# Optimization experiments

Hardware: AMD Instinct MI355X
Metric: run time of the kernel (lower is better)

The kernel has to match this reference:

```python
import jax, jax.numpy as jnp
import numpy as np

D_MODEL = 1024
N_HEAD = 8
STRIDE = 8
HEAD_DIM = D_MODEL // N_HEAD
NEG_INF = jnp.float32(-1e30)  # stand-in for -inf, safe under softmax


def setup_inputs() -> dict:
    key = jax.random.key(0)
    ks = jax.random.split(key, 8)
    B, TGT, SRC = 2, 1024, 8192
    scale = 1.0 / np.sqrt(D_MODEL)
    return {
        "q": jax.random.normal(ks[0], (B, TGT, D_MODEL), jnp.float32),
        "k": jax.random.normal(ks[1], (B, SRC, D_MODEL), jnp.float32),
        "v": jax.random.normal(ks[2], (B, SRC, D_MODEL), jnp.float32),
        "Wq": jax.random.normal(ks[3], (D_MODEL, D_MODEL), jnp.float32) * scale,
        "bq": jnp.zeros((D_MODEL,), jnp.float32),
        "Wk": jax.random.normal(ks[4], (D_MODEL, D_MODEL), jnp.float32) * scale,
        "bk": jnp.zeros((D_MODEL,), jnp.float32),
        "Wv": jax.random.normal(ks[5], (D_MODEL, D_MODEL), jnp.float32) * scale,
        "bv": jnp.zeros((D_MODEL,), jnp.float32),
        "Wo": jax.random.normal(ks[6], (D_MODEL, D_MODEL), jnp.float32) * scale,
        "bo": jnp.zeros((D_MODEL,), jnp.float32),
    }


def _hepos_head_mask(src_len):
    # mask_h[h, j] True where position j is DISALLOWED for head h:
    # (j - h) % stride != 0. If a head would mask everything, unmask j=0
    # (matches the torch fallback; cannot happen when n_head <= stride... it
    # can when h >= stride? here h < n_head <= stride handled generically).
    src_idx = jnp.arange(src_len)  # [src]
    h_idx = jnp.arange(N_HEAD)[:, None]  # [H,1]
    m = ((src_idx[None, :] - h_idx) % STRIDE) != 0  # [H, src]
    all_masked = jnp.all(m, axis=-1, keepdims=True)  # [H,1]
    m = m.at[:, 0].set(jnp.where(all_masked[:, 0], False, m[:, 0]))
    return m


def reference(q, k, v, Wq, bq, Wk, bk, Wv, bv, Wo, bo):
    B, tgt_len, _ = q.shape
    src_len = k.shape[1]
    # projections (torch Linear: x @ W^T + b; here W stored as [d_in, d_out])
    Q = (q @ Wq + bq).reshape(B, tgt_len, N_HEAD, HEAD_DIM)
    K = (k @ Wk + bk).reshape(B, src_len, N_HEAD, HEAD_DIM)
    V = (v @ Wv + bv).reshape(B, src_len, N_HEAD, HEAD_DIM)
    # dense scores [B, H, tgt, src]
    scores = jnp.einsum('bthd,bshd->bhts', Q, K) / np.sqrt(HEAD_DIM)
    head_mask = _hepos_head_mask(src_len)  # [H, src], True -> disallowed
    scores = jnp.where(head_mask[None, :, None, :], NEG_INF, scores)
    attn = jax.nn.softmax(scores, axis=-1)
    out = jnp.einsum('bhts,bshd->bthd', attn, V).reshape(B, tgt_len, D_MODEL)
    return out @ Wo + bo
```

## Files before the change

kernel.cpp:

```cpp
#include <hip/hip_runtime.h>
#include <hip/hip_bf16.h>
#include <stdint.h>

#define DM 1024
#define HD 128
#define NH 8
#define NB 2
#define TGT 1024
#define SRC 8192
#define JPH 1024
#define LOG2E 1.4426950408889634f

typedef __attribute__((ext_vector_type(8))) short bf16x8;
typedef __attribute__((ext_vector_type(4))) float f32x4;

__device__ __forceinline__ unsigned short f2bf(float f) {
  __hip_bfloat16 h = __float2bfloat16(f);
  return __builtin_bit_cast(unsigned short, h);
}

__device__ __forceinline__ void gload_lds16(const void* g, void* l) {
  __builtin_amdgcn_global_load_lds(
      (const __attribute__((address_space(1))) unsigned int*)g,
      (__attribute__((address_space(3))) unsigned int*)l, 16, 0, 0);
}

__global__ __launch_bounds__(256) void wconv_kernel(
    const float* __restrict__ Wq, const float* __restrict__ Wk,
    const float* __restrict__ Wv, const float* __restrict__ Wo,
    unsigned short* __restrict__ WTout) {
  __shared__ float tile[64][65];
  const float* W = (blockIdx.z == 0) ? Wq : (blockIdx.z == 1) ? Wk
                   : (blockIdx.z == 2) ? Wv : Wo;
  unsigned short* WT = WTout + (size_t)blockIdx.z * DM * DM;
  const int k0 = blockIdx.x * 64, n0 = blockIdx.y * 64;
  const int tid = threadIdx.x;
  const int tr = tid >> 4, tc = (tid & 15) * 4;
  for (int it = 0; it < 4; ++it) {
    int r = tr + it * 16;
    float4 vv = *(const float4*)(&W[(size_t)(k0 + r) * DM + n0 + tc]);
    tile[r][tc] = vv.x; tile[r][tc + 1] = vv.y;
    tile[r][tc + 2] = vv.z; tile[r][tc + 3] = vv.w;
  }
  __syncthreads();
  for (int it = 0; it < 4; ++it) {
    int n = tr + it * 16;
    ushort4 o;
    o.x = f2bf(tile[tc + 0][n]); o.y = f2bf(tile[tc + 1][n]);
    o.z = f2bf(tile[tc + 2][n]); o.w = f2bf(tile[tc + 3][n]);
    *(ushort4*)(&WT[(size_t)(n0 + n) * DM + k0 + tc]) = o;
  }
}

__global__ __launch_bounds__(256) void proj_fused_kernel(
    const float* __restrict__ q, const float* __restrict__ k,
    const float* __restrict__ v, const unsigned short* __restrict__ WTall,
    const float* __restrict__ bq, const float* __restrict__ bk,
    const float* __restrict__ bv, unsigned short* __restrict__ Qp,
    unsigned short* __restrict__ Kp, unsigned short* __restrict__ VpT) {
  __shared__ unsigned short Ab[2][128 * 64];
  __shared__ unsigned short Bb[2][128 * 64];
  const int tid = threadIdx.x, lane = tid & 63, w = tid >> 6;
  const int wm = w >> 1, wn = w & 1;
  const int l15 = lane & 15, l4 = lane >> 4;

  const int bid = blockIdx.x;
  const int mode = bid >> 7;
  const int sub = bid & 127;
  const float* Asrc;
  const unsigned short* WT;
  const float* bias;
  int nbase, bh = 0, Mtile;
  if (mode == 0) {
    Asrc = q; WT = WTall; bias = bq;
    Mtile = sub >> 3; nbase = (sub & 7) * 128;
  } else {
    bh = sub >> 3; Mtile = sub & 7;
    nbase = (bh & 7) * 128;
    if (mode == 1) { Asrc = k; WT = WTall + (size_t)DM * DM; bias = bk; }
    else           { Asrc = v; WT = WTall + (size_t)2 * DM * DM; bias = bv; }
  }

  float4 areg[4][2];
  auto loadA = [&](int t) {
    const int kk0 = t * 64;
    for (int p = 0; p < 4; ++p) {
      int r = p * 32 + (tid >> 3);
      size_t grow;
      if (mode == 0) grow = (size_t)(Mtile * 128 + r);
      else grow = (size_t)(bh >> 3) * SRC + (size_t)(bh & 7) +
                  8u * (size_t)(Mtile * 128 + r);
      const float* src = &Asrc[grow * DM + kk0 + (tid & 7) * 8];
      areg[p][0] = *(const float4*)(src);
      areg[p][1] = *(const float4*)(src + 4);
    }
  };
  auto writeA = [&](int buf) {
    for (int p = 0; p < 4; ++p) {
      int r = p * 32 + (tid >> 3);
      bf16x8 pk;
      pk[0] = (short)f2bf(areg[p][0].x); pk[1] = (short)f2bf(areg[p][0].y);
      pk[2] = (short)f2bf(areg[p][0].z); pk[3] = (short)f2bf(areg[p][0].w);
      pk[4] = (short)f2bf(areg[p][1].x); pk[5] = (short)f2bf(areg[p][1].y);
      pk[6] = (short)f2bf(areg[p][1].z); pk[7] = (short)f2bf(areg[p][1].w);
      int off = r * 128 + (((tid & 7) * 16) ^ ((r & 7) << 4));
      *(bf16x8*)((unsigned char*)Ab[buf] + off) = pk;
    }
  };
  auto stageB = [&](int t, int buf) {
    const int kk0 = t * 64;
    for (int it = 0; it < 4; ++it) {
      int gi = w * 4 + it;
      int row = gi * 8 + (lane >> 3);
      const unsigned char* g =
          (const unsigned char*)&WT[(size_t)(nbase + row) * DM + kk0];
      g += ((lane & 7) * 16) ^ ((row & 7) << 4);
      gload_lds16(g, (unsigned char*)Bb[buf] + gi * 1024);
    }
  };

  f32x4 acc[4][4] = {};

  loadA(0);
  stageB(0, 0);
  writeA(0);
  __syncthreads();

  for (int t = 0; t < 16; ++t) {
    const int cur = t & 1;
    if (t < 15) { loadA(t + 1); stageB(t + 1, cur ^ 1); }

    bf16x8 af[4][2], bfr[4][2];
    for (int f = 0; f < 4; ++f)
      for (int kk = 0; kk < 2; ++kk) {
        int ra = wm * 64 + f * 16 + l15;
        int ka = (kk * 64 + l4 * 16) ^ ((ra & 7) << 4);
        af[f][kk] = *(const bf16x8*)((const unsigned char*)Ab[cur] + ra * 128 + ka);
        int rb = wn * 64 + f * 16 + l15;
        int kb = (kk * 64 + l4 * 16) ^ ((rb & 7) << 4);
        bfr[f][kk] = *(const bf16x8*)((const unsigned char*)Bb[cur] + rb * 128 + kb);
      }
    for (int kk = 0; kk < 2; ++kk)
      for (int fm = 0; fm < 4; ++fm)
        for (int fn = 0; fn < 4; ++fn)
          acc[fm][fn] = __builtin_amdgcn_mfma_f32_16x16x32_bf16(
              af[fm][kk], bfr[fn][kk], acc[fm][fn], 0, 0, 0);

    if (t < 15) writeA(cur ^ 1);
    __syncthreads();
  }

  for (int fm = 0; fm < 4; ++fm) {
    for (int fn = 0; fn < 4; ++fn) {
      const int mloc = wm * 64 + fm * 16 + l4 * 4;
      const int nloc = wn * 64 + fn * 16 + l15;
      const float bs = bias[nbase + nloc];
      if (mode == 2) {
        const int d = nloc;
        const int jp = Mtile * 128 + mloc;
        ushort4 o;
        o.x = f2bf(acc[fm][fn][0] + bs); o.y = f2bf(acc[fm][fn][1] + bs);
        o.z = f2bf(acc[fm][fn][2] + bs); o.w = f2bf(acc[fm][fn][3] + bs);
        *(ushort4*)(&VpT[((size_t)bh * HD + d) * JPH + jp]) = o;
      } else if (mode == 1) {
        for (int i = 0; i < 4; ++i) {
          int jp = Mtile * 128 + mloc + i;
          Kp[((size_t)bh * JPH + jp) * HD + nloc] = f2bf(acc[fm][fn][i] + bs);
        }
      } else {
        for (int i = 0; i < 4; ++i) {
          int mg = Mtile * 128 + mloc + i;
          int bb = mg >> 10, tt = mg & 1023;
          int ng = nbase + nloc;
          int h = ng >> 7, d = ng & 127;
          Qp[(((size_t)bb * NH + h) * TGT + tt) * HD + d] =
              f2bf((acc[fm][fn][i] + bs) * 0.08838834764831845f);
        }
      }
    }
  }
}

__global__ __launch_bounds__(256) void attn_kernel(
    const unsigned short* __restrict__ Qp, const unsigned short* __restrict__ Kp,
    const unsigned short* __restrict__ VpT, unsigned short* __restrict__ O) {
  __shared__ unsigned short Klds[64 * 128];
  __shared__ unsigned short Vlds[128 * 64];
  __shared__ unsigned short Plds[4 * 16 * 64];
  const int tid = threadIdx.x, lane = tid & 63, w = tid >> 6;
  const int tq = blockIdx.x, bh = blockIdx.y;
  const int T0 = tq * 64 + w * 16;
  const int l15 = lane & 15, l4 = lane >> 4;

  bf16x8 qf[4];
  {
    const unsigned short* qrow = &Qp[((size_t)bh * TGT + T0 + l15) * HD];
    for (int kf = 0; kf < 4; ++kf)
      qf[kf] = *(const bf16x8*)(&qrow[kf * 32 + l4 * 8]);
  }

  f32x4 acc_o[8] = {};
  float m_run = -INFINITY, l_run = 0.f;

  const unsigned short* kbh = Kp + (size_t)bh * JPH * HD;
  const unsigned short* vbh = VpT + (size_t)bh * HD * JPH;

  for (int jt = 0; jt < 16; ++jt) {
    const int j0 = jt * 64;
    for (int it = 0; it < 4; ++it) {
      int rb = w * 16 + it * 4;
      int row = rb + l4;
      const unsigned char* g =
          (const unsigned char*)(kbh + (size_t)(j0 + row) * HD);
      g += (l15 * 16) ^ ((row & 7) << 4);
      gload_lds16(g, &Klds[rb * 128]);
    }
    for (int it = 0; it < 4; ++it) {
      int rb = w * 32 + it * 8;
      int d = rb + (lane >> 3);
      const unsigned char* g =
          (const unsigned char*)(vbh + (size_t)d * JPH + j0);
      g += ((lane & 7) * 16) ^ ((d & 7) << 4);
      gload_lds16(g, &Vlds[rb * 64]);
    }
    __syncthreads();

    f32x4 acc_s[4] = {};
    for (int jf = 0; jf < 4; ++jf) {
      const int j = jf * 16 + l15;
      for (int kf = 0; kf < 4; ++kf) {
        int byteoff = (j * 256 + (kf * 32 + l4 * 8) * 2) ^ ((j & 7) << 4);
        bf16x8 kfr = *(const bf16x8*)((const unsigned char*)Klds + byteoff);
        acc_s[jf] = __builtin_amdgcn_mfma_f32_16x16x32_bf16(
            kfr, qf[kf], acc_s[jf], 0, 0, 0);
      }
    }

    float pmax = -INFINITY;
    for (int jf = 0; jf < 4; ++jf)
      for (int i = 0; i < 4; ++i) pmax = fmaxf(pmax, acc_s[jf][i]);
    pmax = fmaxf(pmax, __shfl_xor(pmax, 16, 64));
    pmax = fmaxf(pmax, __shfl_xor(pmax, 32, 64));
    const float m_new = fmaxf(m_run, pmax);
    const float alpha = exp2f((m_run - m_new) * LOG2E);
    float psum = 0.f;
    for (int jf = 0; jf < 4; ++jf) {
      float p0 = exp2f((acc_s[jf][0] - m_new) * LOG2E);
      float p1 = exp2f((acc_s[jf][1] - m_new) * LOG2E);
      float p2 = exp2f((acc_s[jf][2] - m_new) * LOG2E);
      float p3 = exp2f((acc_s[jf][3] - m_new) * LOG2E);
      psum += (p0 + p1) + (p2 + p3);
      ushort4 pk;
      pk.x = f2bf(p0); pk.y = f2bf(p1); pk.z = f2bf(p2); pk.w = f2bf(p3);
      int byteoff = (w * 2048 + l15 * 128 + (jf * 16 + l4 * 4) * 2) ^ ((l15 & 7) << 4);
      *(ushort4*)((unsigned char*)Plds + byteoff) = pk;
    }
    psum += __shfl_xor(psum, 16, 64);
    psum += __shfl_xor(psum, 32, 64);
    l_run = l_run * alpha + psum;
    m_run = m_new;

    float alphar[4];
    for (int i = 0; i < 4; ++i)
      alphar[i] = __shfl(alpha, (lane & 48) | (l4 * 4 + i), 64);
    for (int df = 0; df < 8; ++df) {
      acc_o[df][0] *= alphar[0]; acc_o[df][1] *= alphar[1];
      acc_o[df][2] *= alphar[2]; acc_o[df][3] *= alphar[3];
    }

    for (int kf2 = 0; kf2 < 2; ++kf2) {
      int poff = (w * 2048 + l15 * 128 + (kf2 * 32 + l4 * 8) * 2) ^ ((l15 & 7) << 4);
      bf16x8 pf = *(const bf16x8*)((const unsigned char*)Plds + poff);
      for (int df = 0; df < 8; ++df) {
        int d = df * 16 + l15;
        int voff = (d * 128 + (kf2 * 32 + l4 * 8) * 2) ^ ((d & 7) << 4);
        bf16x8 vf = *(const bf16x8*)((const unsigned char*)Vlds + voff);
        acc_o[df] = __builtin_amdgcn_mfma_f32_16x16x32_bf16(
            pf, vf, acc_o[df], 0, 0, 0);
      }
    }
    __syncthreads();
  }

  const float li = 1.0f / l_run;
  float linv[4];
  for (int i = 0; i < 4; ++i)
    linv[i] = __shfl(li, (lane & 48) | (l4 * 4 + i), 64);

  const int b = bh >> 3, h = bh & 7;
  for (int df = 0; df < 8; ++df)
    for (int i = 0; i < 4; ++i) {
      int t = T0 + l4 * 4 + i;
      int d = df * 16 + l15;
      O[((size_t)b * TGT + t) * DM + h * HD + d] = f2bf(acc_o[df][i] * linv[i]);
    }
}

__global__ __launch_bounds__(256) void oproj_kernel(
    const unsigned short* __restrict__ Oin, const unsigned short* __restrict__ WoT,
    const float* __restrict__ bo, float* __restrict__ out) {
  __shared__ unsigned short Ab[2][128 * 64];
  __shared__ unsigned short Bb[2][128 * 64];
  const int tid = threadIdx.x, lane = tid & 63, w = tid >> 6;
  const int wm = w >> 1, wn = w & 1;
  const int n0 = blockIdx.x * 128, m0 = blockIdx.y * 128;
  const int l15 = lane & 15, l4 = lane >> 4;

  auto stage = [&](const unsigned short* src, int rbase, int t, unsigned short* lds) {
    const int kk0 = t * 64;
    for (int it = 0; it < 4; ++it) {
      int gi = w * 4 + it;
      int row = gi * 8 + (lane >> 3);
      const unsigned char* g =
          (const unsigned char*)&src[(size_t)(rbase + row) * DM + kk0];
      g += ((lane & 7) * 16) ^ ((row & 7) << 4);
      gload_lds16(g, (unsigned char*)lds + gi * 1024);
    }
  };

  f32x4 acc[4][4] = {};
  stage(Oin, m0, 0, Ab[0]);
  stage(WoT, n0, 0, Bb[0]);
  __syncthreads();

  for (int t = 0; t < 16; ++t) {
    const int cur = t & 1;
    if (t < 15) {
      stage(Oin, m0, t + 1, Ab[cur ^ 1]);
      stage(WoT, n0, t + 1, Bb[cur ^ 1]);
    }
    bf16x8 af[4][2], bfr[4][2];
    for (int f = 0; f < 4; ++f)
      for (int kk = 0; kk < 2; ++kk) {
        int ra = wm * 64 + f * 16 + l15;
        int ka = (kk * 64 + l4 * 16) ^ ((ra & 7) << 4);
        af[f][kk] = *(const bf16x8*)((const unsigned char*)Ab[cur] + ra * 128 + ka);
        int rb = wn * 64 + f * 16 + l15;
        int kb = (kk * 64 + l4 * 16) ^ ((rb & 7) << 4);
        bfr[f][kk] = *(const bf16x8*)((const unsigned char*)Bb[cur] + rb * 128 + kb);
      }
    for (int kk = 0; kk < 2; ++kk)
      for (int fm = 0; fm < 4; ++fm)
        for (int fn = 0; fn < 4; ++fn)
          acc[fm][fn] = __builtin_amdgcn_mfma_f32_16x16x32_bf16(
              af[fm][kk], bfr[fn][kk], acc[fm][fn], 0, 0, 0);
    __syncthreads();
  }

  for (int fm = 0; fm < 4; ++fm)
    for (int fn = 0; fn < 4; ++fn) {
      int nn = n0 + wn * 64 + fn * 16 + l15;
      float bs = bo[nn];
      for (int i = 0; i < 4; ++i) {
        int mm = m0 + wm * 64 + fm * 16 + l4 * 4 + i;
        out[(size_t)mm * DM + nn] = acc[fm][fn][i] + bs;
      }
    }
}

extern "C" void kernel_launch(void* const* d_in, const int* in_sizes, int n_in,
                              void* d_out, int out_size, void* d_ws,
                              size_t ws_size, hipStream_t stream) {
  const float* q  = (const float*)d_in[0];
  const float* k  = (const float*)d_in[1];
  const float* v  = (const float*)d_in[2];
  const float* Wq = (const float*)d_in[3];
  const float* bq = (const float*)d_in[4];
  const float* Wk = (const float*)d_in[5];
  const float* bk = (const float*)d_in[6];
  const float* Wv = (const float*)d_in[7];
  const float* bv = (const float*)d_in[8];
  const float* Wo = (const float*)d_in[9];
  const float* bo = (const float*)d_in[10];
  float* out = (float*)d_out;

  unsigned short* WT  = (unsigned short*)d_ws;
  unsigned short* Qp  = WT + (size_t)4 * DM * DM;
  unsigned short* Kp  = Qp + (size_t)2 * DM * DM;
  unsigned short* VpT = Kp + (size_t)2 * DM * DM;
  unsigned short* Obf = VpT + (size_t)2 * DM * DM;

  hipLaunchKernelGGL(wconv_kernel, dim3(16, 16, 4), dim3(256), 0, stream,
                     Wq, Wk, Wv, Wo, WT);
  hipLaunchKernelGGL(proj_fused_kernel, dim3(384), dim3(256), 0, stream,
                     q, k, v, WT, bq, bk, bv, Qp, Kp, VpT);
  hipLaunchKernelGGL(attn_kernel, dim3(16, 16), dim3(256), 0, stream,
                     Qp, Kp, VpT, Obf);
  hipLaunchKernelGGL(oproj_kernel, dim3(8, 16), dim3(256), 0, stream,
                     Obf, WT + (size_t)3 * DM * DM, bo, out);
}
```

Before: 114.9 us.

## Halve projection M-tile to 64 rows and stage B through registers

The fused projection kernel now uses 64x128 output tiles instead of 128x128, doubling the grid to 768 blocks and setting launch_bounds occupancy to 3 blocks per CU. The B weight tile is loaded into registers and written to swizzled LDS by hand instead of using global_load_lds. The aim is more blocks across the 256 CUs and more waves per CU to hide latency. The trade-off is lower per-block reuse of the weight tile and extra register-to-LDS traffic for B.

```diff
diff --git a/kernel.cpp b/kernel.cpp
--- a/kernel.cpp
+++ b/kernel.cpp
@@ -52,21 +52,21 @@
   }
 }
 
-__global__ __launch_bounds__(256) void proj_fused_kernel(
+__global__ __launch_bounds__(256, 3) void proj_fused_kernel(
     const float* __restrict__ q, const float* __restrict__ k,
     const float* __restrict__ v, const unsigned short* __restrict__ WTall,
     const float* __restrict__ bq, const float* __restrict__ bk,
     const float* __restrict__ bv, unsigned short* __restrict__ Qp,
     unsigned short* __restrict__ Kp, unsigned short* __restrict__ VpT) {
-  __shared__ unsigned short Ab[2][128 * 64];
+  __shared__ unsigned short Ab[2][64 * 64];
   __shared__ unsigned short Bb[2][128 * 64];
   const int tid = threadIdx.x, lane = tid & 63, w = tid >> 6;
   const int wm = w >> 1, wn = w & 1;
   const int l15 = lane & 15, l4 = lane >> 4;
 
   const int bid = blockIdx.x;
-  const int mode = bid >> 7;
-  const int sub = bid & 127;
+  const int mode = bid >> 8;
+  const int sub = bid & 255;
   const float* Asrc;
   const unsigned short* WT;
   const float* bias;
@@ -75,106 +75,117 @@
     Asrc = q; WT = WTall; bias = bq;
     Mtile = sub >> 3; nbase = (sub & 7) * 128;
   } else {
-    bh = sub >> 3; Mtile = sub & 7;
+    bh = sub >> 4; Mtile = sub & 15;
     nbase = (bh & 7) * 128;
     if (mode == 1) { Asrc = k; WT = WTall + (size_t)DM * DM; bias = bk; }
     else           { Asrc = v; WT = WTall + (size_t)2 * DM * DM; bias = bv; }
   }
 
-  float4 areg[4][2];
-  auto loadA = [&](int t) {
-    const int kk0 = t * 64;
-    for (int p = 0; p < 4; ++p) {
-      int r = p * 32 + (tid >> 3);
-      size_t grow;
-      if (mode == 0) grow = (size_t)(Mtile * 128 + r);
-      else grow = (size_t)(bh >> 3) * SRC + (size_t)(bh & 7) +
-                  8u * (size_t)(Mtile * 128 + r);
-      const float* src = &Asrc[grow * DM + kk0 + (tid & 7) * 8];
-      areg[p][0] = *(const float4*)(src);
-      areg[p][1] = *(const float4*)(src + 4);
-    }
+  const int ar = tid >> 2;
+  const int ac = (tid & 3) * 16;
+  size_t growA;
+  if (mode == 0) growA = (size_t)(Mtile * 64 + ar);
+  else growA = (size_t)(bh >> 3) * SRC + (size_t)(bh & 7) +
+               8u * (size_t)(Mtile * 64 + ar);
+  const float* aptr = &Asrc[growA * DM + ac];
+  const int br = tid >> 1;
+  const int bc = (tid & 1) * 32;
+  const unsigned short* bptr = &WT[(size_t)(nbase + br) * DM + bc];
+
+  float4 aReg[4];
+  uint4 bReg[4];
+
+  auto issue = [&](int t) {
+    const float* ap = aptr + t * 64;
+#pragma unroll
+    for (int i = 0; i < 4; ++i) aReg[i] = *(const float4*)(ap + i * 4);
+    const unsigned short* bp = bptr + t * 64;
+#pragma unroll
+    for (int i = 0; i < 4; ++i) bReg[i] = *(const uint4*)(bp + i * 8);
   };
-  auto writeA = [&](int buf) {
-    for (int p = 0; p < 4; ++p) {
-      int r = p * 32 + (tid >> 3);
+  auto commit = [&](int buf) {
+    unsigned char* abase = (unsigned char*)Ab[buf] + ar * 128;
+#pragma unroll
+    for (int h = 0; h < 2; ++h) {
       bf16x8 pk;
-      pk[0] = (short)f2bf(areg[p][0].x); pk[1] = (short)f2bf(areg[p][0].y);
-      pk[2] = (short)f2bf(areg[p][0].z); pk[3] = (short)f2bf(areg[p][0].w);
-      pk[4] = (short)f2bf(areg[p][1].x); pk[5] = (short)f2bf(areg[p][1].y);
-      pk[6] = (short)f2bf(areg[p][1].z); pk[7] = (short)f2bf(areg[p][1].w);
-      int off = r * 128 + (((tid & 7) * 16) ^ ((r & 7) << 4));
-      *(bf16x8*)((unsigned char*)Ab[buf] + off) = pk;
+      float4 x = aReg[h * 2], y = aReg[h * 2 + 1];
+      pk[0] = (short)f2bf(x.x); pk[1] = (short)f2bf(x.y);
+      pk[2] = (short)f2bf(x.z); pk[3] = (short)f2bf(x.w);
+      pk[4] = (short)f2bf(y.x); pk[5] = (short)f2bf(y.y);
+      pk[6] = (short)f2bf(y.z); pk[7] = (short)f2bf(y.w);
+      int b0 = (ac * 2 + h * 16) ^ ((ar & 7) << 4);
+      *(bf16x8*)(abase + b0) = pk;
+    }
+    unsigned char* bbase = (unsigned char*)Bb[buf] + br * 128;
+#pragma unroll
+    for (int i = 0; i < 4; ++i) {
+      int b0 = (bc * 2 + i * 16) ^ ((br & 7) << 4);
+      *(uint4*)(bbase + b0) = bReg[i];
     }
   };
-  auto stageB = [&](int t, int buf) {
-    const int kk0 = t * 64;
-    for (int it = 0; it < 4; ++it) {
-      int gi = w * 4 + it;
-      int row = gi * 8 + (lane >> 3);
-      const unsigned char* g =
-          (const unsigned char*)&WT[(size_t)(nbase + row) * DM + kk0];
-      g += ((lane & 7) * 16) ^ ((row & 7) << 4);
-      gload_lds16(g, (unsigned char*)Bb[buf] + gi * 1024);
-    }
-  };
-
-  f32x4 acc[4][4] = {};
-
-  loadA(0);
-  stageB(0, 0);
-  writeA(0);
+
+  f32x4 acc[2][4] = {};
+
+  issue(0);
+  commit(0);
   __syncthreads();
 
   for (int t = 0; t < 16; ++t) {
     const int cur = t & 1;
-    if (t < 15) { loadA(t + 1); stageB(t + 1, cur ^ 1); }
-
-    bf16x8 af[4][2], bfr[4][2];
-    for (int f = 0; f < 4; ++f)
-      for (int kk = 0; kk < 2; ++kk) {
-        int ra = wm * 64 + f * 16 + l15;
-        int ka = (kk * 64 + l4 * 16) ^ ((ra & 7) << 4);
-        af[f][kk] = *(const bf16x8*)((const unsigned char*)Ab[cur] + ra * 128 + ka);
-        int rb = wn * 64 + f * 16 + l15;
-        int kb = (kk * 64 + l4 * 16) ^ ((rb & 7) << 4);
-        bfr[f][kk] = *(const bf16x8*)((const unsigned char*)Bb[cur] + rb * 128 + kb);
-      }
-    for (int kk = 0; kk < 2; ++kk)
-      for (int fm = 0; fm < 4; ++fm)
-        for (int fn = 0; fn < 4; ++fn)
-          acc[fm][fn] = __builtin_amdgcn_mfma_f32_16x16x32_bf16(
-              af[fm][kk], bfr[fn][kk], acc[fm][fn], 0, 0, 0);
-
-    if (t < 15) writeA(cur ^ 1);
+    if (t < 15) issue(t + 1);
+#pragma unroll
+    for (int kk = 0; kk < 2; ++kk) {
+      bf16x8 af[2], bfv[4];
+#pragma unroll
+      for (int f = 0; f < 2; ++f) {
+        int ra = wm * 32 + f * 16 + l15;
+        int bo = (kk * 64 + l4 * 16) ^ ((ra & 7) << 4);
+        af[f] = *(const bf16x8*)((const unsigned char*)Ab[cur] + ra * 128 + bo);
+      }
+#pragma unroll
+      for (int g = 0; g < 4; ++g) {
+        int rb = wn * 64 + g * 16 + l15;
+        int bo = (kk * 64 + l4 * 16) ^ ((rb & 7) << 4);
+        bfv[g] = *(const bf16x8*)((const unsigned char*)Bb[cur] + rb * 128 + bo);
+      }
+#pragma unroll
+      for (int f = 0; f < 2; ++f)
+#pragma unroll
+        for (int g = 0; g < 4; ++g)
+          acc[f][g] = __builtin_amdgcn_mfma_f32_16x16x32_bf16(
+              af[f], bfv[g], acc[f][g], 0, 0, 0);
+    }
+    if (t < 15) commit(cur ^ 1);
     __syncthreads();
   }
 
-  for (int fm = 0; fm < 4; ++fm) {
-    for (int fn = 0; fn < 4; ++fn) {
-      const int mloc = wm * 64 + fm * 16 + l4 * 4;
-      const int nloc = wn * 64 + fn * 16 + l15;
+#pragma unroll
+  for (int f = 0; f < 2; ++f) {
+#pragma unroll
+    for (int g = 0; g < 4; ++g) {
+      const int mloc = wm * 32 + f * 16 + l4 * 4;
+      const int nloc = wn * 64 + g * 16 + l15;
       const float bs = bias[nbase + nloc];
       if (mode == 2) {
         const int d = nloc;
-        const int jp = Mtile * 128 + mloc;
+        const int jp = Mtile * 64 + mloc;
         ushort4 o;
-        o.x = f2bf(acc[fm][fn][0] + bs); o.y = f2bf(acc[fm][fn][1] + bs);
-        o.z = f2bf(acc[fm][fn][2] + bs); o.w = f2bf(acc[fm][fn][3] + bs);
+        o.x = f2bf(acc[f][g][0] + bs); o.y = f2bf(acc[f][g][1] + bs);
+        o.z = f2bf(acc[f][g][2] + bs); o.w = f2bf(acc[f][g][3] + bs);
         *(ushort4*)(&VpT[((size_t)bh * HD + d) * JPH + jp]) = o;
       } else if (mode == 1) {
         for (int i = 0; i < 4; ++i) {
-          int jp = Mtile * 128 + mloc + i;
-          Kp[((size_t)bh * JPH + jp) * HD + nloc] = f2bf(acc[fm][fn][i] + bs);
+          int jp = Mtile * 64 + mloc + i;
+          Kp[((size_t)bh * JPH + jp) * HD + nloc] = f2bf(acc[f][g][i] + bs);
         }
       } else {
         for (int i = 0; i < 4; ++i) {
-          int mg = Mtile * 128 + mloc + i;
+          int mg = Mtile * 64 + mloc + i;
           int bb = mg >> 10, tt = mg & 1023;
           int ng = nbase + nloc;
           int h = ng >> 7, d = ng & 127;
           Qp[(((size_t)bb * NH + h) * TGT + tt) * HD + d] =
-              f2bf((acc[fm][fn][i] + bs) * 0.08838834764831845f);
+              f2bf((acc[f][g][i] + bs) * 0.08838834764831845f);
         }
       }
     }
@@ -382,7 +393,7 @@
 
   hipLaunchKernelGGL(wconv_kernel, dim3(16, 16, 4), dim3(256), 0, stream,
                      Wq, Wk, Wv, Wo, WT);
-  hipLaunchKernelGGL(proj_fused_kernel, dim3(384), dim3(256), 0, stream,
+  hipLaunchKernelGGL(proj_fused_kernel, dim3(768), dim3(256), 0, stream,
                      q, k, v, WT, bq, bk, bv, Qp, Kp, VpT);
   hipLaunchKernelGGL(attn_kernel, dim3(16, 16), dim3(256), 0, stream,
                      Qp, Kp, VpT, Obf);
```

New measurement: 130.2 us. 1.13x slower.

## Deepen A-tile register prefetch in projection kernel with explicit waitcnt barriers

Applied to the files above, without the earlier changes.

Restructures the projection GEMM main loop to prefetch A tiles two steps ahead into two alternating register sets. It replaces __syncthreads with explicit s_waitcnt vmcnt/lgkmcnt plus s_barrier and sched_barrier, and fully unrolls the loops. It also adds a min-blocks-per-CU hint of 2 to launch_bounds. The aim is to hide global-load latency behind MFMA work, at the cost of more VGPR pressure from the doubled register buffers and fragile hand-written wait counts.

```diff
diff --git a/kernel.cpp b/kernel.cpp
--- a/kernel.cpp
+++ b/kernel.cpp
@@ -52,7 +52,7 @@
   }
 }
 
-__global__ __launch_bounds__(256) void proj_fused_kernel(
+__global__ __launch_bounds__(256, 2) void proj_fused_kernel(
     const float* __restrict__ q, const float* __restrict__ k,
     const float* __restrict__ v, const unsigned short* __restrict__ WTall,
     const float* __restrict__ bq, const float* __restrict__ bk,
@@ -81,34 +81,47 @@
     else           { Asrc = v; WT = WTall + (size_t)2 * DM * DM; bias = bv; }
   }
 
-  float4 areg[4][2];
-  auto loadA = [&](int t) {
+  const int arow = tid >> 3;
+  const int acol = (tid & 7) * 8;
+  const float* aptr;
+  {
+    size_t grow0;
+    if (mode == 0) grow0 = (size_t)(Mtile * 128);
+    else grow0 = (size_t)(bh >> 3) * SRC + (size_t)(bh & 7);
+    aptr = Asrc;
+    (void)grow0;
+  }
+
+  auto issueA = [&](int t, float4 (&R)[4][2]) {
     const int kk0 = t * 64;
+#pragma unroll
     for (int p = 0; p < 4; ++p) {
-      int r = p * 32 + (tid >> 3);
+      int r = p * 32 + arow;
       size_t grow;
       if (mode == 0) grow = (size_t)(Mtile * 128 + r);
       else grow = (size_t)(bh >> 3) * SRC + (size_t)(bh & 7) +
                   8u * (size_t)(Mtile * 128 + r);
-      const float* src = &Asrc[grow * DM + kk0 + (tid & 7) * 8];
-      areg[p][0] = *(const float4*)(src);
-      areg[p][1] = *(const float4*)(src + 4);
+      const float* src = &Asrc[grow * DM + kk0 + acol];
+      R[p][0] = *(const float4*)(src);
+      R[p][1] = *(const float4*)(src + 4);
     }
   };
-  auto writeA = [&](int buf) {
+  auto commitA = [&](float4 (&R)[4][2], int buf) {
+#pragma unroll
     for (int p = 0; p < 4; ++p) {
-      int r = p * 32 + (tid >> 3);
+      int r = p * 32 + arow;
       bf16x8 pk;
-      pk[0] = (short)f2bf(areg[p][0].x); pk[1] = (short)f2bf(areg[p][0].y);
-      pk[2] = (short)f2bf(areg[p][0].z); pk[3] = (short)f2bf(areg[p][0].w);
-      pk[4] = (short)f2bf(areg[p][1].x); pk[5] = (short)f2bf(areg[p][1].y);
-      pk[6] = (short)f2bf(areg[p][1].z); pk[7] = (short)f2bf(areg[p][1].w);
-      int off = r * 128 + (((tid & 7) * 16) ^ ((r & 7) << 4));
+      pk[0] = (short)f2bf(R[p][0].x); pk[1] = (short)f2bf(R[p][0].y);
+      pk[2] = (short)f2bf(R[p][0].z); pk[3] = (short)f2bf(R[p][0].w);
+      pk[4] = (short)f2bf(R[p][1].x); pk[5] = (short)f2bf(R[p][1].y);
+      pk[6] = (short)f2bf(R[p][1].z); pk[7] = (short)f2bf(R[p][1].w);
+      int off = r * 128 + ((acol * 2) ^ ((r & 7) << 4));
       *(bf16x8*)((unsigned char*)Ab[buf] + off) = pk;
     }
   };
   auto stageB = [&](int t, int buf) {
     const int kk0 = t * 64;
+#pragma unroll
     for (int it = 0; it < 4; ++it) {
       int gi = w * 4 + it;
       int row = gi * 8 + (lane >> 3);
@@ -120,37 +133,59 @@
   };
 
   f32x4 acc[4][4] = {};
-
-  loadA(0);
+  float4 aR0[4][2], aR1[4][2];
+
   stageB(0, 0);
-  writeA(0);
-  __syncthreads();
-
-  for (int t = 0; t < 16; ++t) {
-    const int cur = t & 1;
-    if (t < 15) { loadA(t + 1); stageB(t + 1, cur ^ 1); }
+  issueA(0, aR0);
+  issueA(1, aR1);
+  commitA(aR0, 0);
+  asm volatile("s_waitcnt vmcnt(8) lgkmcnt(0)" ::: "memory");
+  __builtin_amdgcn_s_barrier();
+  __builtin_amdgcn_sched_barrier(0);
+
+  auto body = [&](int T, int CUR, float4 (&RC)[4][2], float4 (&RN)[4][2]) {
+    if (T + 1 < 16) stageB(T + 1, CUR ^ 1);
+    if (T + 2 < 16) issueA(T + 2, RC);
 
     bf16x8 af[4][2], bfr[4][2];
+#pragma unroll
     for (int f = 0; f < 4; ++f)
+#pragma unroll
       for (int kk = 0; kk < 2; ++kk) {
         int ra = wm * 64 + f * 16 + l15;
         int ka = (kk * 64 + l4 * 16) ^ ((ra & 7) << 4);
-        af[f][kk] = *(const bf16x8*)((const unsigned char*)Ab[cur] + ra * 128 + ka);
+        af[f][kk] = *(const bf16x8*)((const unsigned char*)Ab[CUR] + ra * 128 + ka);
         int rb = wn * 64 + f * 16 + l15;
         int kb = (kk * 64 + l4 * 16) ^ ((rb & 7) << 4);
-        bfr[f][kk] = *(const bf16x8*)((const unsigned char*)Bb[cur] + rb * 128 + kb);
-      }
+        bfr[f][kk] = *(const bf16x8*)((const unsigned char*)Bb[CUR] + rb * 128 + kb);
+      }
+#pragma unroll
     for (int kk = 0; kk < 2; ++kk)
+#pragma unroll
       for (int fm = 0; fm < 4; ++fm)
+#pragma unroll
         for (int fn = 0; fn < 4; ++fn)
           acc[fm][fn] = __builtin_amdgcn_mfma_f32_16x16x32_bf16(
               af[fm][kk], bfr[fn][kk], acc[fm][fn], 0, 0, 0);
 
-    if (t < 15) writeA(cur ^ 1);
-    __syncthreads();
-  }
-
+    if (T + 1 < 16) commitA(RN, CUR ^ 1);
+
+    if (T + 2 < 16)
+      asm volatile("s_waitcnt vmcnt(8) lgkmcnt(0)" ::: "memory");
+    else
+      asm volatile("s_waitcnt vmcnt(0) lgkmcnt(0)" ::: "memory");
+    __builtin_amdgcn_s_barrier();
+    __builtin_amdgcn_sched_barrier(0);
+  };
+
+  for (int tt = 0; tt < 16; tt += 2) {
+    body(tt, 0, aR0, aR1);
+    body(tt + 1, 1, aR1, aR0);
+  }
+
+#pragma unroll
   for (int fm = 0; fm < 4; ++fm) {
+#pragma unroll
     for (int fn = 0; fn < 4; ++fn) {
       const int mloc = wm * 64 + fm * 16 + l4 * 4;
       const int nloc = wn * 64 + fn * 16 + l15;
@@ -170,10 +205,10 @@
       } else {
         for (int i = 0; i < 4; ++i) {
           int mg = Mtile * 128 + mloc + i;
-          int bb = mg >> 10, tt = mg & 1023;
+          int bb = mg >> 10, tt2 = mg & 1023;
           int ng = nbase + nloc;
           int h = ng >> 7, d = ng & 127;
-          Qp[(((size_t)bb * NH + h) * TGT + tt) * HD + d] =
+          Qp[(((size_t)bb * NH + h) * TGT + tt2) * HD + d] =
               f2bf((acc[fm][fn][i] + bs) * 0.08838834764831845f);
         }
       }
```

Result: faster. 107.3 us (-6.7%).
